# Kernel tuning notes

Measured on AMD Instinct MI355X. Metric: run time of the kernel, lower is better.

The kernel has to match this reference:

```python
import jax, jax.numpy as jnp
import numpy as np

M = 16            # num_frequencies
DIM = 512         # dim_input
B = 32768         # flattened batch
H = M + 1         # raw complex table side
N = 2 * M + 1     # autocorrelated table side
NPAR = H * H      # (m+1)^2


def setup_inputs() -> dict:
    key = jax.random.key(0)
    k1, k2, k3 = jax.random.split(key, 3)
    inputs = jax.random.normal(k1, (B, DIM), dtype=jnp.float32)
    targets = jax.random.uniform(k2, (B, 2), dtype=jnp.float32)  # points in [0,1) subset of [-1,1]^2
    # nn.init.normal_(weight, 0.01) => mean=0.01, std=1.0 ; bias zeros
    W = jax.random.normal(k3, (2 * NPAR, DIM), dtype=jnp.float32) + 0.01
    b = jnp.zeros((2 * NPAR,), dtype=jnp.float32)
    return {"inputs": inputs, "targets": targets, "W": W, "b": b}


def reference(inputs, targets, W, b):
    # Linear -> unconstrained complex (m+1)x(m+1) table per sample
    p = inputs @ W.T + b                                   # (B, 2*NPAR)
    real = p[:, :NPAR].reshape(-1, H, H)
    imag = p[:, NPAR:].reshape(-1, H, H)
    seq = jax.lax.complex(real, imag)                      # (B, H, H) complex64

    # 2D linear autocorrelation r[tau] = sum_i seq[i+tau] * conj(seq[i]),
    # tau in [-M, M]^2, via zero-padded FFT (equivalent to the grouped conv2d).
    F = jnp.fft.fft2(seq, s=(N, N))                        # (B, N, N)
    ac = jnp.fft.ifft2(F * jnp.conj(F))                    # circular autocorr
    ac = jnp.roll(ac, (M, M), axis=(-2, -1))               # index a -> lag a-M

    # Normalize so C[0,0] (= centre) equals 1/4 => unit mass on [-1,1]^2
    centre = ac[:, M, M].real                              # sum |seq|^2 > 0
    C = ac / (4.0 * centre)[:, None, None]                 # (B, N, N)

    # Evaluate f(x,y) = sum_{kx,ky} C * exp(i*pi*(kx*x + ky*y))
    k = jnp.arange(-M, M + 1, dtype=jnp.float32)
    kx, ky = jnp.meshgrid(k, k, indexing='xy')             # (N, N)
    tx = targets[:, 0][:, None, None]
    ty = targets[:, 1][:, None, None]
    phase = kx[None] * tx + ky[None] * ty                  # (B, N, N)
    exps = jnp.exp(1j * jnp.pi * phase)
    pdf = jnp.einsum('bij,bij->b', C, exps).real           # (B,)
    return pdf
```

## Files before the change

### kernel.cpp

```cpp
#include <hip/hip_runtime.h>

#define NPARC 289
#define NOUT  578
#define DIMK  512
#define BATCH 32768

typedef __bf16 bf16x8 __attribute__((ext_vector_type(8)));
typedef float floatx4 __attribute__((ext_vector_type(4)));

__device__ __forceinline__ unsigned short f2bf(float f) {
    unsigned u = __float_as_uint(f);
    u = (u + 0x7fffu + ((u >> 16) & 1u)) >> 16;
    return (unsigned short)u;
}

__global__ void prep_w(const float* __restrict__ W, unsigned short* __restrict__ Wp) {
    int wid = threadIdx.x >> 6;
    int lane = threadIdx.x & 63;
    int slot = blockIdx.x * 4 + wid;
    int k = lane * 8;
    unsigned short v[8];
    if (slot < NOUT) {
        int o = (slot & 1) ? NPARC + (slot >> 1) : (slot >> 1);
        const float* src = W + (size_t)o * DIMK + k;
        #pragma unroll
        for (int j = 0; j < 8; ++j) v[j] = f2bf(src[j]);
    } else {
        #pragma unroll
        for (int j = 0; j < 8; ++j) v[j] = 0;
    }
    int ct = slot >> 4;
    int ks = k >> 5;
    int ln = (((k >> 3) & 3) << 4) + (slot & 15);
    uint4 o4;
    o4.x = (unsigned)v[0] | ((unsigned)v[1] << 16);
    o4.y = (unsigned)v[2] | ((unsigned)v[3] << 16);
    o4.z = (unsigned)v[4] | ((unsigned)v[5] << 16);
    o4.w = (unsigned)v[6] | ((unsigned)v[7] << 16);
    *(uint4*)(Wp + (size_t)((ct * 16 + ks) * 64 + ln) * 8) = o4;
}

__global__ __launch_bounds__(512, 2) void fused_kernel(
    const float* __restrict__ inputs, const float* __restrict__ targets,
    const float* __restrict__ bias, const unsigned short* __restrict__ Wp,
    float* __restrict__ out)
{
    __shared__ __align__(16) unsigned short buf[2][64][16][8];
    __shared__ float R[8][64][3];
    const int tid  = threadIdx.x;
    const int base = blockIdx.x * 64;
    const int wid  = tid >> 6;
    const int lane = tid & 63;
    const int quad = lane >> 4;
    const int lcol = lane & 15;
    const int ct0  = wid * 5;

    const int ss = tid >> 3;
    const int su = tid & 7;
    const float4* sp = (const float4*)(inputs + (size_t)(base + ss) * DIMK + su * 16);
    const int slot0 = (2 * su)     ^ (ss & 7);
    const int slot1 = (2 * su + 1) ^ (ss & 7);

    float4 g0, g1, g2, g3;

#define WRITE_STAGE(nb) do {                                                  \
    union { __bf16 h[8]; uint4 u; } c0_, c1_;                                 \
    c0_.h[0]=(__bf16)g0.x; c0_.h[1]=(__bf16)g0.y;                             \
    c0_.h[2]=(__bf16)g0.z; c0_.h[3]=(__bf16)g0.w;                             \
    c0_.h[4]=(__bf16)g1.x; c0_.h[5]=(__bf16)g1.y;                             \
    c0_.h[6]=(__bf16)g1.z; c0_.h[7]=(__bf16)g1.w;                             \
    c1_.h[0]=(__bf16)g2.x; c1_.h[1]=(__bf16)g2.y;                             \
    c1_.h[2]=(__bf16)g2.z; c1_.h[3]=(__bf16)g2.w;                             \
    c1_.h[4]=(__bf16)g3.x; c1_.h[5]=(__bf16)g3.y;                             \
    c1_.h[6]=(__bf16)g3.z; c1_.h[7]=(__bf16)g3.w;                             \
    *(uint4*)&buf[nb][ss][slot0][0] = c0_.u;                                  \
    *(uint4*)&buf[nb][ss][slot1][0] = c1_.u;                                  \
} while (0)

#define LDBS(dst, bb, kss)                                                    \
    { _Pragma("unroll") for (int st_ = 0; st_ < 4; ++st_)                     \
        dst[st_] = *(const bf16x8*)&buf[bb][st_ * 16 + lcol]                  \
                       [((kss) * 4 + quad) ^ (lcol & 7)][0]; }

#define LDAW(dst, ksg)                                                        \
    { _Pragma("unroll") for (int t5_ = 0; t5_ < 5; ++t5_)                     \
        dst[t5_] = Wf[((size_t)(ct0 + t5_) * 16 + (ksg)) * 64 + lane]; }

#define DOMFMA(aww, bss)                                                      \
    { _Pragma("unroll") for (int t5_ = 0; t5_ < 5; ++t5_)                     \
        { _Pragma("unroll") for (int st_ = 0; st_ < 4; ++st_)                 \
            acc[t5_][st_] = __builtin_amdgcn_mfma_f32_16x16x32_bf16(          \
                aww[t5_], bss[st_], acc[t5_][st_], 0, 0, 0); } }

    g0 = sp[0]; g1 = sp[1]; g2 = sp[2]; g3 = sp[3];
    WRITE_STAGE(0);
    __syncthreads();

    float xs[4], ys[4];
    #pragma unroll
    for (int st = 0; st < 4; ++st) {
        float2 t2 = *(const float2*)(targets + 2 * (base + st * 16 + lcol));
        xs[st] = 0.5f * t2.x;
        ys[st] = 0.5f * t2.y;
    }

    floatx4 acc[5][4];
    #pragma unroll
    for (int t5 = 0; t5 < 5; ++t5)
        #pragma unroll
        for (int st = 0; st < 4; ++st) acc[t5][st] = (floatx4){0.f, 0.f, 0.f, 0.f};

    const bf16x8* Wf = (const bf16x8*)Wp;

    bf16x8 bsP[4], awP[5], bsQ[4], awQ[5];
    LDBS(bsP, 0, 0);
    LDAW(awP, 0);

    #pragma unroll
    for (int kt = 0; kt < 4; ++kt) {
        const int cur = kt & 1;
        if (kt < 3) {
            g0 = sp[(kt + 1) * 32 + 0];
            g1 = sp[(kt + 1) * 32 + 1];
            g2 = sp[(kt + 1) * 32 + 2];
            g3 = sp[(kt + 1) * 32 + 3];
        }
        #pragma unroll
        for (int ks = 0; ks < 4; ++ks) {
            const int ksg = kt * 4 + ks;
            if (ksg & 1) {
                if (ks < 3)      { LDBS(bsP, cur, ks + 1); LDAW(awP, ksg + 1); }
                else if (kt < 3) { LDAW(awP, ksg + 1); }
                DOMFMA(awQ, bsQ);
            } else {
                if (ks < 3)      { LDBS(bsQ, cur, ks + 1); LDAW(awQ, ksg + 1); }
                else if (kt < 3) { LDAW(awQ, ksg + 1); }
                DOMFMA(awP, bsP);
            }
        }
        __syncthreads();
        if (kt < 3) {
            WRITE_STAGE(1 - cur);
            __syncthreads();
            LDBS(bsP, 1 - cur, 0);
        }
    }

    float pd[4]  = {0.f, 0.f, 0.f, 0.f};
    float pr[4]  = {0.f, 0.f, 0.f, 0.f};
    float pim[4] = {0.f, 0.f, 0.f, 0.f};

    #pragma unroll
    for (int t5 = 0; t5 < 5; ++t5)
        #pragma unroll
        for (int p = 0; p < 2; ++p) {
            int colw = (ct0 + t5) * 16 + quad * 4 + 2 * p;
            if (colw < NOUT) {
                int j = colw >> 1;
                int r = j / 17;
                int c = j - r * 17;
                float cf = (float)c, rf = (float)r;
                float be = bias[j];
                float bo = bias[j + NPARC];
                #pragma unroll
                for (int st = 0; st < 4; ++st) {
                    float ve = acc[t5][st][2 * p]     + be;
                    float vo = acc[t5][st][2 * p + 1] + bo;
                    float u = fmaf(cf, xs[st], rf * ys[st]);
                    u = __builtin_amdgcn_fractf(u);
                    float sn = __builtin_amdgcn_sinf(u);
                    float cs = __builtin_amdgcn_cosf(u);
                    pd[st]  = fmaf(ve, ve, pd[st]);
                    pd[st]  = fmaf(vo, vo, pd[st]);
                    pr[st]  = fmaf(ve, cs, pr[st]);
                    pr[st]  = fmaf(-vo, sn, pr[st]);
                    pim[st] = fmaf(ve, sn, pim[st]);
                    pim[st] = fmaf(vo, cs, pim[st]);
                }
            }
        }

    #pragma unroll
    for (int d = 16; d < 64; d <<= 1)
        #pragma unroll
        for (int st = 0; st < 4; ++st) {
            pd[st]  += __shfl_xor(pd[st], d, 64);
            pr[st]  += __shfl_xor(pr[st], d, 64);
            pim[st] += __shfl_xor(pim[st], d, 64);
        }

    if (lane < 16) {
        #pragma unroll
        for (int st = 0; st < 4; ++st) {
            int sl = st * 16 + lane;
            R[wid][sl][0] = pd[st];
            R[wid][sl][1] = pr[st];
            R[wid][sl][2] = pim[st];
        }
    }
    __syncthreads();

    if (tid < 64) {
        float sd = 0.f, sr = 0.f, si = 0.f;
        #pragma unroll
        for (int w = 0; w < 8; ++w) {
            sd += R[w][tid][0];
            sr += R[w][tid][1];
            si += R[w][tid][2];
        }
        out[base + tid] = (sr * sr + si * si) / (4.0f * sd);
    }
#undef WRITE_STAGE
#undef LDBS
#undef LDAW
#undef DOMFMA
}

extern "C" void kernel_launch(void* const* d_in, const int* in_sizes, int n_in,
                              void* d_out, int out_size, void* d_ws, size_t ws_size,
                              hipStream_t stream) {
    const float* inputs  = (const float*)d_in[0];
    const float* targets = (const float*)d_in[1];
    const float* W       = (const float*)d_in[2];
    const float* bias    = (const float*)d_in[3];
    unsigned short* Wp   = (unsigned short*)d_ws;

    prep_w<<<160, 256, 0, stream>>>(W, Wp);
    fused_kernel<<<BATCH / 64, 512, 0, stream>>>(inputs, targets, bias, Wp, (float*)d_out);
}
```

Before: 121.2 us.

## Stream fp32 inputs into LDS via global_load_lds and convert to bf16 after LDS read

Replaces the register-staged global load plus bf16 conversion and LDS store with direct global-to-LDS async loads of raw fp32 input tiles into an XOR-swizzled double buffer. The bf16 conversion moves to after the LDS read, just before each MFMA group. The K loop is manually unrolled with ping-pong register sets, sched barriers and setprio around the MFMA bursts. This removes VGPR staging and the extra sync on the write path, at the cost of doubling LDS footprint (fp32) and LDS read bandwidth, and doing the conversion redundantly per wave.

New measurement: 120.3 us. No clear change (-0.8%).

```diff
diff --git a/kernel.cpp b/kernel.cpp
--- a/kernel.cpp
+++ b/kernel.cpp
@@ -45,7 +45,7 @@
     const float* __restrict__ bias, const unsigned short* __restrict__ Wp,
     float* __restrict__ out)
 {
-    __shared__ __align__(16) unsigned short buf[2][64][16][8];
+    __shared__ __align__(16) float buf[2][64 * 128];
     __shared__ float R[8][64][3];
     const int tid  = threadIdx.x;
     const int base = blockIdx.x * 64;
@@ -54,47 +54,99 @@
     const int quad = lane >> 4;
     const int lcol = lane & 15;
     const int ct0  = wid * 5;
-
-    const int ss = tid >> 3;
-    const int su = tid & 7;
-    const float4* sp = (const float4*)(inputs + (size_t)(base + ss) * DIMK + su * 16);
-    const int slot0 = (2 * su)     ^ (ss & 7);
-    const int slot1 = (2 * su + 1) ^ (ss & 7);
-
-    float4 g0, g1, g2, g3;
-
-#define WRITE_STAGE(nb) do {                                                  \
-    union { __bf16 h[8]; uint4 u; } c0_, c1_;                                 \
-    c0_.h[0]=(__bf16)g0.x; c0_.h[1]=(__bf16)g0.y;                             \
-    c0_.h[2]=(__bf16)g0.z; c0_.h[3]=(__bf16)g0.w;                             \
-    c0_.h[4]=(__bf16)g1.x; c0_.h[5]=(__bf16)g1.y;                             \
-    c0_.h[6]=(__bf16)g1.z; c0_.h[7]=(__bf16)g1.w;                             \
-    c1_.h[0]=(__bf16)g2.x; c1_.h[1]=(__bf16)g2.y;                             \
-    c1_.h[2]=(__bf16)g2.z; c1_.h[3]=(__bf16)g2.w;                             \
-    c1_.h[4]=(__bf16)g3.x; c1_.h[5]=(__bf16)g3.y;                             \
-    c1_.h[6]=(__bf16)g3.z; c1_.h[7]=(__bf16)g3.w;                             \
-    *(uint4*)&buf[nb][ss][slot0][0] = c0_.u;                                  \
-    *(uint4*)&buf[nb][ss][slot1][0] = c1_.u;                                  \
+    const bf16x8* Wf = (const bf16x8*)Wp;
+
+#define STAGE(nb, kt) do {                                                    \
+    _Pragma("unroll") for (int j_ = 0; j_ < 4; ++j_) {                        \
+        int I_ = wid * 4 + j_;                                                \
+        int r_ = I_ * 2 + (lane >> 5);                                        \
+        int cl_ = (lane & 31) ^ (r_ & 15);                                    \
+        const float* g_ = inputs + (size_t)(base + r_) * DIMK + (kt) * 128 + cl_ * 4; \
+        void* l_ = (char*)&buf[nb][0] + I_ * 1024;                            \
+        __builtin_amdgcn_global_load_lds(                                     \
+            (const __attribute__((address_space(1))) unsigned int*)g_,        \
+            (__attribute__((address_space(3))) unsigned int*)l_, 16, 0, 0);   \
+    }                                                                         \
 } while (0)
 
-#define LDBS(dst, bb, kss)                                                    \
-    { _Pragma("unroll") for (int st_ = 0; st_ < 4; ++st_)                     \
-        dst[st_] = *(const bf16x8*)&buf[bb][st_ * 16 + lcol]                  \
-                       [((kss) * 4 + quad) ^ (lcol & 7)][0]; }
+#define LDRAW(R_, nb, kl) do {                                                \
+    _Pragma("unroll") for (int st_ = 0; st_ < 4; ++st_) {                     \
+        int s_ = st_ * 16 + lcol;                                             \
+        int cb_ = (kl) * 8 + quad * 2;                                        \
+        const char* p_ = (const char*)&buf[nb][0] + s_ * 512;                 \
+        R_[2 * st_]     = *(const floatx4*)(p_ + ((cb_)     ^ (s_ & 15)) * 16); \
+        R_[2 * st_ + 1] = *(const floatx4*)(p_ + ((cb_ + 1) ^ (s_ & 15)) * 16); \
+    }                                                                         \
+} while (0)
 
 #define LDAW(dst, ksg)                                                        \
     { _Pragma("unroll") for (int t5_ = 0; t5_ < 5; ++t5_)                     \
         dst[t5_] = Wf[((size_t)(ct0 + t5_) * 16 + (ksg)) * 64 + lane]; }
 
-#define DOMFMA(aww, bss)                                                      \
-    { _Pragma("unroll") for (int t5_ = 0; t5_ < 5; ++t5_)                     \
+#define KS(nb, ksg, RU, RP, PF, AWU, AWP) do {                                \
+    if (PF) LDRAW(RP, nb, ((ksg) & 3) + 1);                                   \
+    if ((ksg) < 15) LDAW(AWP, (ksg) + 1);                                     \
+    bf16x8 bsv[4];                                                            \
+    _Pragma("unroll") for (int st_ = 0; st_ < 4; ++st_) {                     \
+        union { __bf16 h[8]; bf16x8 v; } cu_;                                 \
+        cu_.h[0] = (__bf16)RU[2 * st_][0];     cu_.h[1] = (__bf16)RU[2 * st_][1]; \
+        cu_.h[2] = (__bf16)RU[2 * st_][2];     cu_.h[3] = (__bf16)RU[2 * st_][3]; \
+        cu_.h[4] = (__bf16)RU[2 * st_ + 1][0]; cu_.h[5] = (__bf16)RU[2 * st_ + 1][1]; \
+        cu_.h[6] = (__bf16)RU[2 * st_ + 1][2]; cu_.h[7] = (__bf16)RU[2 * st_ + 1][3]; \
+        bsv[st_] = cu_.v;                                                     \
+    }                                                                         \
+    __builtin_amdgcn_sched_barrier(0);                                        \
+    __builtin_amdgcn_s_setprio(1);                                            \
+    _Pragma("unroll") for (int t5_ = 0; t5_ < 5; ++t5_)                       \
         { _Pragma("unroll") for (int st_ = 0; st_ < 4; ++st_)                 \
             acc[t5_][st_] = __builtin_amdgcn_mfma_f32_16x16x32_bf16(          \
-                aww[t5_], bss[st_], acc[t5_][st_], 0, 0, 0); } }
-
-    g0 = sp[0]; g1 = sp[1]; g2 = sp[2]; g3 = sp[3];
-    WRITE_STAGE(0);
-    __syncthreads();
+                AWU[t5_], bsv[st_], acc[t5_][st_], 0, 0, 0); }                \
+    __builtin_amdgcn_s_setprio(0);                                            \
+    __builtin_amdgcn_sched_barrier(0);                                        \
+} while (0)
+
+    floatx4 acc[5][4];
+    #pragma unroll
+    for (int t5 = 0; t5 < 5; ++t5)
+        #pragma unroll
+        for (int st = 0; st < 4; ++st) acc[t5][st] = (floatx4){0.f, 0.f, 0.f, 0.f};
+
+    bf16x8 aw0[5], aw1[5];
+    floatx4 rA[8], rB[8];
+
+    STAGE(0, 0);
+    LDAW(aw0, 0);
+    __syncthreads();
+
+    STAGE(1, 1);
+    LDRAW(rA, 0, 0);
+    KS(0, 0,  rA, rB, 1, aw0, aw1);
+    KS(0, 1,  rB, rA, 1, aw1, aw0);
+    KS(0, 2,  rA, rB, 1, aw0, aw1);
+    KS(0, 3,  rB, rA, 0, aw1, aw0);
+    __syncthreads();
+
+    STAGE(0, 2);
+    LDRAW(rA, 1, 0);
+    KS(1, 4,  rA, rB, 1, aw0, aw1);
+    KS(1, 5,  rB, rA, 1, aw1, aw0);
+    KS(1, 6,  rA, rB, 1, aw0, aw1);
+    KS(1, 7,  rB, rA, 0, aw1, aw0);
+    __syncthreads();
+
+    STAGE(1, 3);
+    LDRAW(rA, 0, 0);
+    KS(0, 8,  rA, rB, 1, aw0, aw1);
+    KS(0, 9,  rB, rA, 1, aw1, aw0);
+    KS(0, 10, rA, rB, 1, aw0, aw1);
+    KS(0, 11, rB, rA, 0, aw1, aw0);
+    __syncthreads();
+
+    LDRAW(rA, 1, 0);
+    KS(1, 12, rA, rB, 1, aw0, aw1);
+    KS(1, 13, rB, rA, 1, aw1, aw0);
+    KS(1, 14, rA, rB, 1, aw0, aw1);
+    KS(1, 15, rB, rA, 0, aw1, aw0);
 
     float xs[4], ys[4];
     #pragma unroll
@@ -104,48 +156,6 @@
         ys[st] = 0.5f * t2.y;
     }
 
-    floatx4 acc[5][4];
-    #pragma unroll
-    for (int t5 = 0; t5 < 5; ++t5)
-        #pragma unroll
-        for (int st = 0; st < 4; ++st) acc[t5][st] = (floatx4){0.f, 0.f, 0.f, 0.f};
-
-    const bf16x8* Wf = (const bf16x8*)Wp;
-
-    bf16x8 bsP[4], awP[5], bsQ[4], awQ[5];
-    LDBS(bsP, 0, 0);
-    LDAW(awP, 0);
-
-    #pragma unroll
-    for (int kt = 0; kt < 4; ++kt) {
-        const int cur = kt & 1;
-        if (kt < 3) {
-            g0 = sp[(kt + 1) * 32 + 0];
-            g1 = sp[(kt + 1) * 32 + 1];
-            g2 = sp[(kt + 1) * 32 + 2];
-            g3 = sp[(kt + 1) * 32 + 3];
-        }
-        #pragma unroll
-        for (int ks = 0; ks < 4; ++ks) {
-            const int ksg = kt * 4 + ks;
-            if (ksg & 1) {
-                if (ks < 3)      { LDBS(bsP, cur, ks + 1); LDAW(awP, ksg + 1); }
-                else if (kt < 3) { LDAW(awP, ksg + 1); }
-                DOMFMA(awQ, bsQ);
-            } else {
-                if (ks < 3)      { LDBS(bsQ, cur, ks + 1); LDAW(awQ, ksg + 1); }
-                else if (kt < 3) { LDAW(awQ, ksg + 1); }
-                DOMFMA(awP, bsP);
-            }
-        }
-        __syncthreads();
-        if (kt < 3) {
-            WRITE_STAGE(1 - cur);
-            __syncthreads();
-            LDBS(bsP, 1 - cur, 0);
-        }
-    }
-
     float pd[4]  = {0.f, 0.f, 0.f, 0.f};
     float pr[4]  = {0.f, 0.f, 0.f, 0.f};
     float pim[4] = {0.f, 0.f, 0.f, 0.f};
@@ -156,12 +166,12 @@
         for (int p = 0; p < 2; ++p) {
             int colw = (ct0 + t5) * 16 + quad * 4 + 2 * p;
             if (colw < NOUT) {
-                int j = colw >> 1;
-                int r = j / 17;
-                int c = j - r * 17;
+                int jj = colw >> 1;
+                int r = jj / 17;
+                int c = jj - r * 17;
                 float cf = (float)c, rf = (float)r;
-                float be = bias[j];
-                float bo = bias[j + NPARC];
+                float be = bias[jj];
+                float bo = bias[jj + NPARC];
                 #pragma unroll
                 for (int st = 0; st < 4; ++st) {
                     float ve = acc[t5][st][2 * p]     + be;
@@ -210,10 +220,10 @@
         }
         out[base + tid] = (sr * sr + si * si) / (4.0f * sd);
     }
-#undef WRITE_STAGE
-#undef LDBS
+#undef STAGE
+#undef LDRAW
 #undef LDAW
-#undef DOMFMA
+#undef KS
 }
 
 extern "C" void kernel_launch(void* const* d_in, const int* in_sizes, int n_in,
```
